# Optimization experiments

Hardware: AMD Instinct MI355X
Metric: run time of the kernel (lower is better)

The kernel has to match this reference:

```python
import jax, jax.numpy as jnp
import numpy as np

# SMPL constants and module defaults
NV, NF, T, S = 6890, 13776, 3, 256
NEAR, FAR = 0.1, 25.0
VIEW_ANGLE = 30.0
EYE = np.array([0.0, 0.0, -(1.0 / np.tan(np.radians(VIEW_ANGLE)) + 1.0)], np.float32)
AMB_INT, DIR_INT = 1.0, 0.0
AMB_COL = np.array([1.0, 1.0, 1.0], np.float32)
DIR_COL = np.array([1.0, 1.0, 1.0], np.float32)
LIGHT_DIR = np.array([0.0, 1.0, 0.0], np.float32)
BG = np.array([0.0, 0.0, 0.0], np.float32)
CHUNK = 128  # faces processed per z-buffer scan step


def _coords(t):
    # create_coords: (2, T*T) barycentric-style grid over [0,1]^2 (torch meshgrid 'ij')
    step = 1.0 / (t - 1) if t > 1 else 1.0
    ab = np.arange(0.0, 1.0 + step * 0.5, step, dtype=np.float32)
    xv, yv = np.meshgrid(ab, ab, indexing='ij')
    return jnp.asarray(np.stack([xv.ravel(), yv.ravel()], 0))

COORDS = _coords(T)


def _grid_sample(img, grid):
    # F.grid_sample: bilinear, zeros padding, align_corners=False
    # img (B,C,H,W), grid (B,N,M,2) in [-1,1] -> (B,C,N,M)
    Bc, C, H, W = img.shape
    gx = (grid[..., 0] + 1.0) * (W * 0.5) - 0.5
    gy = (grid[..., 1] + 1.0) * (H * 0.5) - 0.5
    x0 = jnp.floor(gx)
    y0 = jnp.floor(gy)
    fx = gx - x0
    fy = gy - y0

    def tap(xi, yi, w):
        valid = (xi >= 0) & (xi < W) & (yi >= 0) & (yi < H)
        xc = jnp.clip(xi, 0, W - 1).astype(jnp.int32)
        yc = jnp.clip(yi, 0, H - 1).astype(jnp.int32)
        v = jax.vmap(lambda im, y, x: im[:, y, x])(img, yc, xc)  # (B,C,N,M)
        return v * (w * valid)[:, None]

    return (tap(x0, y0, (1 - fx) * (1 - fy)) + tap(x0 + 1, y0, fx * (1 - fy))
            + tap(x0, y0 + 1, (1 - fx) * fy) + tap(x0 + 1, y0 + 1, fx * fy))


def _rasterize_one(f3, tex):
    # f3: (NF,3,3) camera-space face vertices (x,y in [-1,1] screen, z depth)
    # tex: (NF,T,T,T,3) per-face texture cube. Z-buffer rasterization (NMR-style,
    # CCW front faces only, perspective-correct depth and texture weights).
    F = f3.shape[0]
    pad = (-F) % CHUNK
    f3p = jnp.concatenate([f3, jnp.zeros((pad, 3, 3), f3.dtype)], 0)
    nc = f3p.shape[0] // CHUNK
    chunks = f3p.reshape(nc, CHUNK, 3, 3)
    bases = jnp.arange(nc, dtype=jnp.int32) * CHUNK
    yi, xi = jnp.meshgrid(jnp.arange(S), jnp.arange(S), indexing='ij')
    px = ((2.0 * xi.ravel() + 1.0 - S) / S).astype(f3.dtype)  # (P,)
    py = ((2.0 * yi.ravel() + 1.0 - S) / S).astype(f3.dtype)
    P = S * S

    @jax.checkpoint
    def step(carry, inp):
        zbuf, fid, wbuf = carry
        base, fc = inp
        vx = fc[:, :, 0][..., None]  # (C,3,1)
        vy = fc[:, :, 1][..., None]
        vz = fc[:, :, 2]             # (C,3)
        x0, x1, x2 = vx[:, 0], vx[:, 1], vx[:, 2]
        y0, y1, y2 = vy[:, 0], vy[:, 1], vy[:, 2]
        det = (x1 - x0) * (y2 - y0) - (y1 - y0) * (x2 - x0)  # (C,1)
        e0 = (x1 - px) * (y2 - py) - (y1 - py) * (x2 - px)   # (C,P)
        e1 = (x2 - px) * (y0 - py) - (y2 - py) * (x0 - px)
        e2 = (x0 - px) * (y1 - py) - (y0 - py) * (x1 - px)
        den = jnp.where(jnp.abs(det) > 1e-10, det, 1.0)
        b0, b1, b2 = e0 / den, e1 / den, e2 / den
        zs = jnp.where(jnp.abs(vz) > 1e-8, vz, 1.0)  # (C,3)
        inv_z = b0 / zs[:, 0:1] + b1 / zs[:, 1:2] + b2 / zs[:, 2:3]
        inv_z = jnp.where(jnp.abs(inv_z) > 1e-8, inv_z, 1.0)
        zp = 1.0 / inv_z  # perspective-correct depth at pixel
        inside = (det > 1e-10) & (e0 >= 0) & (e1 >= 0) & (e2 >= 0)
        valid = inside & (zp > NEAR) & (zp < FAR)
        zm = jnp.where(valid, zp, jnp.inf)
        best = jnp.argmin(zm, axis=0)  # (P,)
        bz = jnp.take_along_axis(zm, best[None], 0)[0]
        w = jnp.stack([jnp.take_along_axis(b0, best[None], 0)[0],
                       jnp.take_along_axis(b1, best[None], 0)[0],
                       jnp.take_along_axis(b2, best[None], 0)[0]], -1)  # (P,3)
        zv = zs[best]  # (P,3)
        bzf = jnp.where(jnp.isfinite(bz), bz, 0.0)
        wpc = (w / zv) * bzf[:, None]  # perspective-correct barycentric
        upd = bz < zbuf
        zbuf = jnp.where(upd, bz, zbuf)
        fid = jnp.where(upd, base + best.astype(jnp.int32), fid)
        wbuf = jnp.where(upd[:, None], wpc, wbuf)
        return (zbuf, fid, wbuf), None

    init = (jnp.full((P,), jnp.inf, f3.dtype),
            jnp.full((P,), -1, jnp.int32),
            jnp.zeros((P, 3), f3.dtype))
    (zbuf, fid, wbuf), _ = jax.lax.scan(step, init, (bases, chunks))

    # trilinear texture-cube sampling at barycentric position
    fg = fid >= 0
    fidc = jnp.clip(fid, 0, F - 1)
    pos = jnp.clip(wbuf, 0.0, 1.0) * (T - 1)  # (P,3)
    i0 = jnp.clip(jnp.floor(pos), 0, max(T - 2, 0)).astype(jnp.int32)
    fr = jnp.clip(pos - i0, 0.0, 1.0)
    col = jnp.zeros((P, 3), f3.dtype)
    for d0 in (0, 1):
        for d1 in (0, 1):
            for d2 in (0, 1):
                wgt = ((fr[:, 0] if d0 else 1 - fr[:, 0])
                       * (fr[:, 1] if d1 else 1 - fr[:, 1])
                       * (fr[:, 2] if d2 else 1 - fr[:, 2]))
                c = tex[fidc,
                        jnp.minimum(i0[:, 0] + d0, T - 1),
                        jnp.minimum(i0[:, 1] + d1, T - 1),
                        jnp.minimum(i0[:, 2] + d2, T - 1)]  # (P,3)
                col = col + wgt[:, None] * c
    img = jnp.where(fg[:, None], col, jnp.asarray(BG, f3.dtype))
    return img.reshape(S, S, 3).transpose(2, 0, 1)  # (3,S,S)


def _forward(cam, vertices, uv_imgs, faces):
    B = cam.shape[0]
    # --- dynamic_sampler: orthographic projection + per-face barycentric UV grid ---
    pts2d = cam[:, None, 0:1] * (vertices[:, :, :2] + cam[:, None, 1:3])  # (B,NV,2)
    f2pts = pts2d[:, faces]                                               # (B,NF,3,2)
    v2 = f2pts[:, :, 2]
    mat = jnp.stack([f2pts[:, :, 0] - v2, f2pts[:, :, 1] - v2], axis=-1)  # (B,NF,2,2)
    sampler = jnp.einsum('bfik,kt->bfti', mat, COORDS) + v2[:, :, None, :]
    sampler = jnp.clip(sampler, -1.0, 1.0)                                # (B,NF,T*T,2)
    # --- extract_tex ---
    tex = _grid_sample(uv_imgs, sampler)                                  # (B,3,NF,T*T)
    tex = tex.reshape(B, 3, NF, T, T).transpose(0, 2, 3, 4, 1)            # (B,NF,T,T,3)
    textures = jnp.repeat(tex[:, :, :, :, None, :], T, axis=4)            # (B,NF,T,T,T,3)
    # --- lighting (defaults: ambient=1, directional=0 -> identity; kept general) ---
    fverts = vertices[:, faces]  # (B,NF,3,3)
    n = jnp.cross(fverts[:, :, 1] - fverts[:, :, 0], fverts[:, :, 2] - fverts[:, :, 0])
    n = n / (jnp.linalg.norm(n, axis=-1, keepdims=True) + 1e-10)
    ldir = jnp.asarray(LIGHT_DIR / np.linalg.norm(LIGHT_DIR))
    cos = jax.nn.relu(n @ ldir)
    light = AMB_INT * jnp.asarray(AMB_COL) + DIR_INT * jnp.asarray(DIR_COL) * cos[..., None]
    tex_lit = textures * light[:, :, None, None, None, :]
    # --- projection (y flipped) + look_at ---
    proj = jnp.concatenate([pts2d[..., 0:1], -pts2d[..., 1:2], vertices[:, :, 2:3]], -1)
    eye = jnp.asarray(EYE)
    z_ax = -eye / jnp.linalg.norm(eye)
    x_ax = jnp.cross(jnp.array([0.0, 1.0, 0.0], proj.dtype), z_ax)
    x_ax = x_ax / jnp.linalg.norm(x_ax)
    y_ax = jnp.cross(z_ax, x_ax)
    R = jnp.stack([x_ax, y_ax, z_ax])  # (3,3)
    vcam = (proj - eye) @ R.T
    f3 = vcam[:, faces]  # (B,NF,3,3)
    images = jax.vmap(_rasterize_one)(f3, tex_lit)  # (B,3,S,S)
    return images, textures


def setup_inputs() -> dict:
    key = jax.random.key(0)
    k1, k2, k3, k4 = jax.random.split(key, 4)
    cam = jax.random.uniform(k1, (1, 3), dtype=jnp.float32)
    vertices = jax.random.normal(k2, (1, NV, 3), dtype=jnp.float32)
    uv_imgs = jax.random.uniform(k3, (1, 3, 256, 256), dtype=jnp.float32)
    faces = jax.random.randint(k4, (NF, 3), 0, NV, dtype=jnp.int32)
    return {"cam": cam, "vertices": vertices, "uv_imgs": uv_imgs, "faces": faces}


def reference(cam, vertices, uv_imgs, faces):
    return _forward(cam, vertices, uv_imgs, faces)
```

## Files before the change

kernel.cpp:

```cpp
#include <hip/hip_runtime.h>

#define NVERT 6890
#define NFACE 13776
#define SS 256
#define NPIX (SS*SS)
#define TILE 8
#define NSB 256
#define SPLIT 16
#define SEGLEN 861
#define SENTINEL 0xFFFFFFFFFFFFFFFFULL
#define ZBASE 0x3D000000u
#define EYEZ 2.7320508075688776f

#define OFF_KEYS 0u
#define OFF_FD   524288u
#define OFF_HIST 1405952u
#define OFF_CURS 1406976u
#define OFF_TD2  1408000u

static __device__ __forceinline__ unsigned int zbucket(unsigned int zmb) {
  return (zmb > ZBASE) ? min(255u, (zmb - ZBASE) >> 19) : 0u;
}

static __device__ __forceinline__ float edgef(float ax, float ay, float bx, float by,
                                              float px, float py) {
  return __fsub_rn(__fmul_rn(__fsub_rn(ax, px), __fsub_rn(by, py)),
                   __fmul_rn(__fsub_rn(ay, py), __fsub_rn(bx, px)));
}

__global__ __launch_bounds__(256) void tex_k(const float* __restrict__ cam,
                                             const float* __restrict__ verts,
                                             const int* __restrict__ faces,
                                             const float* __restrict__ uv,
                                             float* __restrict__ out_tex) {
  int tid = blockIdx.x * 256 + threadIdx.x;
  if (tid >= NFACE * 9) return;
  int f = tid / 9, t = tid - f * 9;
  int ti = t / 3, tj = t - ti * 3;
  float xt = 0.5f * (float)ti;
  float yt = 0.5f * (float)tj;
  float c0 = cam[0], c1 = cam[1], c2 = cam[2];
  int ia = faces[f*3+0], ib = faces[f*3+1], ic = faces[f*3+2];
  float ax = __fmul_rn(c0, __fadd_rn(verts[ia*3+0], c1));
  float ay = __fmul_rn(c0, __fadd_rn(verts[ia*3+1], c2));
  float bx = __fmul_rn(c0, __fadd_rn(verts[ib*3+0], c1));
  float by = __fmul_rn(c0, __fadd_rn(verts[ib*3+1], c2));
  float cx = __fmul_rn(c0, __fadd_rn(verts[ic*3+0], c1));
  float cy = __fmul_rn(c0, __fadd_rn(verts[ic*3+1], c2));
  float sx = (ax - cx) * xt + (bx - cx) * yt + cx;
  float sy = (ay - cy) * xt + (by - cy) * yt + cy;
  sx = fminf(fmaxf(sx, -1.f), 1.f);
  sy = fminf(fmaxf(sy, -1.f), 1.f);
  float gx = (sx + 1.f) * 128.f - 0.5f;
  float gy = (sy + 1.f) * 128.f - 0.5f;
  float x0f = floorf(gx), y0f = floorf(gy);
  float fx = gx - x0f, fy = gy - y0f;
  int x0 = (int)x0f, y0 = (int)y0f;
  float r = 0.f, g = 0.f, b = 0.f;
  #pragma unroll
  for (int dy = 0; dy < 2; ++dy) {
    #pragma unroll
    for (int dx = 0; dx < 2; ++dx) {
      int xi = x0 + dx, yi = y0 + dy;
      if (xi >= 0 && xi < SS && yi >= 0 && yi < SS) {
        float w = (dx ? fx : 1.f - fx) * (dy ? fy : 1.f - fy);
        int base = yi * SS + xi;
        r += w * uv[base];
        g += w * uv[NPIX + base];
        b += w * uv[2 * NPIX + base];
      }
    }
  }
  float* ot = out_tex + f * 81 + ti * 27 + tj * 9;
  #pragma unroll
  for (int kk = 0; kk < 3; ++kk) {
    ot[kk*3+0] = r; ot[kk*3+1] = g; ot[kk*3+2] = b;
  }
}

__global__ __launch_bounds__(256) void setup_k(const float* __restrict__ cam,
                                               const float* __restrict__ verts,
                                               const int* __restrict__ faces,
                                               float* __restrict__ fd,
                                               unsigned int* __restrict__ hist) {
  int f = blockIdx.x * 256 + threadIdx.x;
  if (f >= NFACE) return;
  float* fp = fd + (size_t)f * 16;
  float c0 = cam[0], c1 = cam[1], c2 = cam[2];
  int ia = faces[f*3+0], ib = faces[f*3+1], ic = faces[f*3+2];
  float x0 =  __fmul_rn(c0, __fadd_rn(verts[ia*3+0], c1));
  float y0 = -__fmul_rn(c0, __fadd_rn(verts[ia*3+1], c2));
  float z0 =  __fadd_rn(verts[ia*3+2], EYEZ);
  float x1 =  __fmul_rn(c0, __fadd_rn(verts[ib*3+0], c1));
  float y1 = -__fmul_rn(c0, __fadd_rn(verts[ib*3+1], c2));
  float z1 =  __fadd_rn(verts[ib*3+2], EYEZ);
  float x2 =  __fmul_rn(c0, __fadd_rn(verts[ic*3+0], c1));
  float y2 = -__fmul_rn(c0, __fadd_rn(verts[ic*3+1], c2));
  float z2 =  __fadd_rn(verts[ic*3+2], EYEZ);
  float det = edgef(x1, y1, x2, y2, x0, y0);
  unsigned int tilepack = 0x000000FFu;
  if (det > 1e-10f) {
    float mnx = fminf(x0, fminf(x1, x2)), mxx = fmaxf(x0, fmaxf(x1, x2));
    float mny = fminf(y0, fminf(y1, y2)), mxy = fmaxf(y0, fmaxf(y1, y2));
    int xlo = max((int)floorf((mnx * 256.f + 255.f) * 0.5f) - 2, 0);
    int xhi = min((int)ceilf ((mxx * 256.f + 255.f) * 0.5f) + 2, SS - 1);
    int ylo = max((int)floorf((mny * 256.f + 255.f) * 0.5f) - 2, 0);
    int yhi = min((int)ceilf ((mxy * 256.f + 255.f) * 0.5f) + 2, SS - 1);
    if (xlo <= xhi && ylo <= yhi)
      tilepack = (unsigned int)(xlo >> 3) | ((unsigned int)(ylo >> 3) << 8)
               | ((unsigned int)(xhi >> 3) << 16) | ((unsigned int)(yhi >> 3) << 24);
  }
  float rz0 = (fabsf(z0) > 1e-8f) ? z0 : 1.0f;
  float rz1 = (fabsf(z1) > 1e-8f) ? z1 : 1.0f;
  float rz2 = (fabsf(z2) > 1e-8f) ? z2 : 1.0f;
  float minrz = fminf(fminf(fabsf(rz0), fabsf(rz1)), fabsf(rz2));
  unsigned int flag = (minrz < 0.05f) ? 1u : 0u;
  unsigned int zmb = 0u;
  if (flag == 0u) {
    float mn = fminf(fminf(rz0, rz1), rz2);
    if (mn > 0.f) zmb = __float_as_uint(mn * 0.999f);
  }
  fp[0] = x0;  fp[1] = y0;  fp[2] = x1;  fp[3] = y1;
  fp[4] = x2;  fp[5] = y2;  fp[6] = rz0; fp[7] = rz1;
  fp[8] = rz2; fp[9] = det;
  fp[10] = __fdiv_rn(1.0f, det * rz0);
  fp[11] = __fdiv_rn(1.0f, det * rz1);
  fp[12] = __fdiv_rn(1.0f, det * rz2);
  fp[13] = __uint_as_float((unsigned int)f | (flag << 24));
  fp[14] = __uint_as_float(tilepack);
  fp[15] = __uint_as_float(zmb);
  atomicAdd(&hist[zbucket(zmb)], 1u);
}

__global__ __launch_bounds__(256) void scatter_k(const float* __restrict__ fd,
                                                 const unsigned int* __restrict__ hist,
                                                 unsigned int* __restrict__ curs,
                                                 uint4* __restrict__ td2) {
  __shared__ unsigned int bsh[256];
  int tid = threadIdx.x;
  unsigned int v = hist[tid];
  bsh[tid] = v;
  __syncthreads();
  for (int off = 1; off < 256; off <<= 1) {
    unsigned int t = (tid >= off) ? bsh[tid - off] : 0u;
    __syncthreads();
    bsh[tid] += t;
    __syncthreads();
  }
  int f = blockIdx.x * 256 + tid;
  if (f >= NFACE) return;
  const float* fp = fd + (size_t)f * 16;
  unsigned int tilepack = __float_as_uint(fp[14]);
  unsigned int zmb      = __float_as_uint(fp[15]);
  unsigned int b = zbucket(zmb);
  unsigned int slot = (bsh[b] - hist[b]) + atomicAdd(&curs[b], 1u);
  unsigned int pos = (slot & 15u) * SEGLEN + (slot >> 4);
  td2[pos] = make_uint4(tilepack, zmb, (unsigned int)f, 0u);
}

__global__ __launch_bounds__(256) void tile_k(const float* __restrict__ fd,
                                              const uint4* __restrict__ td2,
                                              unsigned long long* __restrict__ keys) {
  __shared__ unsigned short idx_s[4][256];
  __shared__ unsigned int cnt_s[4];
  __shared__ unsigned int wmax_s[4];
  int sb  = blockIdx.x & (NSB - 1);
  int seg = blockIdx.x >> 8;
  int tid = threadIdx.x;
  int w = tid >> 6, lane = tid & 63;
  int sbx = sb & 15, sby = sb >> 4;
  int tx = sbx * 2 + (w & 1);
  int ty = sby * 2 + (w >> 1);
  int xx = tx * TILE + (lane & 7);
  int yy = ty * TILE + (lane >> 3);
  float px = (float)(2 * xx + 1 - SS) * (1.0f / 256.0f);
  float py = (float)(2 * yy + 1 - SS) * (1.0f / 256.0f);
  int p = yy * SS + xx;
  unsigned long long best = SENTINEL;
  unsigned long long lastw = SENTINEL;
  const uint4* tseg = td2 + (size_t)seg * SEGLEN;

  for (int base = 0; base < SEGLEN; base += 256) {
    unsigned int gz = (unsigned int)(keys[p] >> 32);
    unsigned int kz = min((unsigned int)(best >> 32), gz);
    unsigned int bh = kz;
    #pragma unroll
    for (int o = 32; o > 0; o >>= 1)
      bh = max(bh, (unsigned int)__shfl_xor((int)bh, o, 64));
    __syncthreads();
    if (lane == 0) wmax_s[w] = bh;
    if (tid < 4) cnt_s[tid] = 0;
    __syncthreads();
    unsigned int bm = max(max(wmax_s[0], wmax_s[1]), max(wmax_s[2], wmax_s[3]));
    unsigned int z0 = tseg[base].y;
    unsigned int b0 = zbucket(z0);
    unsigned int lb = b0 ? (ZBASE + (b0 << 19)) : 0u;
    if (lb > bm) break;
    int fi = base + tid;
    if (fi < SEGLEN) {
      uint4 t2 = tseg[fi];
      unsigned int tp = t2.x, zmb = t2.y;
      int tx0 = (int)(tp & 255u),         ty0 = (int)((tp >> 8) & 255u);
      int tx1 = (int)((tp >> 16) & 255u), ty1 = (int)(tp >> 24);
      #pragma unroll
      for (int q = 0; q < 4; ++q) {
        int qtx = sbx * 2 + (q & 1);
        int qty = sby * 2 + (q >> 1);
        if (qtx >= tx0 && qtx <= tx1 && qty >= ty0 && qty <= ty1
            && zmb <= wmax_s[q]) {
          unsigned int slot = atomicAdd(&cnt_s[q], 1u);
          idx_s[q][slot] = (unsigned short)t2.z;
        }
      }
    }
    __syncthreads();
    int m = (int)cnt_s[w];
    for (int j = 0; j < m; ++j) {
      int f2 = __builtin_amdgcn_readfirstlane((int)idx_s[w][j]);
      const float4* fr = (const float4*)(fd + (size_t)f2 * 16);
      float4 A  = fr[0];
      float4 Bv = fr[1];
      float4 Cv = fr[2];
      float4 Dv = fr[3];
      unsigned int zmb = __float_as_uint(Dv.w);
      if (zmb > kz) continue;
      float e0 = edgef(A.z, A.w, Bv.x, Bv.y, px, py);
      float e1 = edgef(Bv.x, Bv.y, A.x, A.y, px, py);
      float e2 = edgef(A.x, A.y, A.z, A.w, px, py);
      if (e0 >= 0.f && e1 >= 0.f && e2 >= 0.f) {
        float inva = __fmaf_rn(e0, Cv.z, __fmaf_rn(e1, Cv.w, e2 * Dv.x));
        float zc = __uint_as_float(kz);
        unsigned int w13 = __float_as_uint(Dv.y);
        bool pass = (kz >= 0x7F800000u)
                  | ((w13 >> 24) != 0u) | (inva * zc > 0.998f) | (fabsf(inva) < 1e-4f);
        if (pass) {
          float rz0 = Bv.z, rz1 = Bv.w, rz2 = Cv.x, det = Cv.y;
          float b0f = __fdiv_rn(e0, det);
          float b1f = __fdiv_rn(e1, det);
          float b2f = __fdiv_rn(e2, det);
          float inv = __fadd_rn(__fadd_rn(__fdiv_rn(b0f, rz0), __fdiv_rn(b1f, rz1)),
                                __fdiv_rn(b2f, rz2));
          if (!(fabsf(inv) > 1e-8f)) inv = 1.0f;
          float zp = __fdiv_rn(1.0f, inv);
          if (zp > 0.1f && zp < 25.0f) {
            unsigned long long key =
                ((unsigned long long)__float_as_uint(zp) << 32)
                | (w13 & 0x00FFFFFFu);
            if (key < best) {
              best = key;
              kz = min(kz, (unsigned int)(best >> 32));
            }
          }
        }
      }
    }
    if (best != lastw && (unsigned int)(best >> 32) <= gz) {
      atomicMin(&keys[p], best);
      lastw = best;
    }
  }
}

__global__ __launch_bounds__(256) void resolve_k(const float* __restrict__ cam,
                                                 const float* __restrict__ verts,
                                                 const int* __restrict__ faces,
                                                 const unsigned long long* __restrict__ keys,
                                                 const float* __restrict__ out_tex,
                                                 float* __restrict__ out_img) {
  int p = blockIdx.x * 256 + threadIdx.x;
  if (p >= NPIX) return;
  unsigned long long k = keys[p];
  float c0v = 0.f, c1v = 0.f, c2v = 0.f;
  if (k != SENTINEL) {
    int f = (int)(unsigned int)(k & 0x00FFFFFFULL);
    float bz = __uint_as_float((unsigned int)(k >> 32));
    int xx = p & (SS - 1), yy = p >> 8;
    float px = (float)(2 * xx + 1 - SS) * (1.0f / 256.0f);
    float py = (float)(2 * yy + 1 - SS) * (1.0f / 256.0f);
    float c0 = cam[0], c1 = cam[1], c2 = cam[2];
    int ia = faces[f*3+0], ib = faces[f*3+1], ic = faces[f*3+2];
    float x0 =  __fmul_rn(c0, __fadd_rn(verts[ia*3+0], c1));
    float y0 = -__fmul_rn(c0, __fadd_rn(verts[ia*3+1], c2));
    float z0 =  __fadd_rn(verts[ia*3+2], EYEZ);
    float x1 =  __fmul_rn(c0, __fadd_rn(verts[ib*3+0], c1));
    float y1 = -__fmul_rn(c0, __fadd_rn(verts[ib*3+1], c2));
    float z1 =  __fadd_rn(verts[ib*3+2], EYEZ);
    float x2 =  __fmul_rn(c0, __fadd_rn(verts[ic*3+0], c1));
    float y2 = -__fmul_rn(c0, __fadd_rn(verts[ic*3+1], c2));
    float z2 =  __fadd_rn(verts[ic*3+2], EYEZ);
    float det = edgef(x1, y1, x2, y2, x0, y0);
    float e0 = edgef(x1, y1, x2, y2, px, py);
    float e1 = edgef(x2, y2, x0, y0, px, py);
    float e2 = edgef(x0, y0, x1, y1, px, py);
    float b0 = __fdiv_rn(e0, det);
    float b1 = __fdiv_rn(e1, det);
    float b2 = __fdiv_rn(e2, det);
    float rz0 = (fabsf(z0) > 1e-8f) ? z0 : 1.0f;
    float rz1 = (fabsf(z1) > 1e-8f) ? z1 : 1.0f;
    float rz2 = (fabsf(z2) > 1e-8f) ? z2 : 1.0f;
    float w0 = __fmul_rn(__fdiv_rn(b0, rz0), bz);
    float w1 = __fmul_rn(__fdiv_rn(b1, rz1), bz);
    float w2 = __fmul_rn(__fdiv_rn(b2, rz2), bz);
    float pos0 = fminf(fmaxf(w0, 0.f), 1.f) * 2.f;
    float pos1 = fminf(fmaxf(w1, 0.f), 1.f) * 2.f;
    float pos2 = fminf(fmaxf(w2, 0.f), 1.f) * 2.f;
    float i0f = fminf(fmaxf(floorf(pos0), 0.f), 1.f);
    float i1f = fminf(fmaxf(floorf(pos1), 0.f), 1.f);
    float i2f = fminf(fmaxf(floorf(pos2), 0.f), 1.f);
    float fr0 = fminf(fmaxf(__fsub_rn(pos0, i0f), 0.f), 1.f);
    float fr1 = fminf(fmaxf(__fsub_rn(pos1, i1f), 0.f), 1.f);
    float fr2 = fminf(fmaxf(__fsub_rn(pos2, i2f), 0.f), 1.f);
    int i00 = (int)i0f, i01 = (int)i1f;
    #pragma unroll
    for (int d0 = 0; d0 < 2; ++d0) {
      float wa = d0 ? fr0 : __fsub_rn(1.f, fr0);
      #pragma unroll
      for (int d1 = 0; d1 < 2; ++d1) {
        float wb = d1 ? fr1 : __fsub_rn(1.f, fr1);
        int a = min(i00 + d0, 2);
        int b = min(i01 + d1, 2);
        const float* tp = &out_tex[f * 81 + a * 27 + b * 9];
        float wab = __fmul_rn(wa, wb);
        #pragma unroll
        for (int d2 = 0; d2 < 2; ++d2) {
          float wc = d2 ? fr2 : __fsub_rn(1.f, fr2);
          float wgt = __fmul_rn(wab, wc);
          c0v = __fadd_rn(c0v, __fmul_rn(wgt, tp[0]));
          c1v = __fadd_rn(c1v, __fmul_rn(wgt, tp[1]));
          c2v = __fadd_rn(c2v, __fmul_rn(wgt, tp[2]));
        }
      }
    }
  }
  out_img[p]          = c0v;
  out_img[NPIX + p]   = c1v;
  out_img[2*NPIX + p] = c2v;
}

extern "C" void kernel_launch(void* const* d_in, const int* in_sizes, int n_in,
                              void* d_out, int out_size, void* d_ws, size_t ws_size,
                              hipStream_t stream) {
  const float* cam   = (const float*)d_in[0];
  const float* verts = (const float*)d_in[1];
  const float* uv    = (const float*)d_in[2];
  const int*   faces = (const int*)d_in[3];
  float* out_img = (float*)d_out;
  float* out_tex = (float*)d_out + 3 * NPIX;

  char* ws = (char*)d_ws;
  unsigned long long* keys = (unsigned long long*)(ws + OFF_KEYS);
  float* fd          = (float*)(ws + OFF_FD);
  unsigned int* hist = (unsigned int*)(ws + OFF_HIST);
  unsigned int* curs = (unsigned int*)(ws + OFF_CURS);
  uint4* td2         = (uint4*)(ws + OFF_TD2);

  hipMemsetAsync(keys, 0xFF, (size_t)NPIX * 8, stream);
  hipMemsetAsync(hist, 0, 2048, stream);
  setup_k<<<(NFACE + 255) / 256, 256, 0, stream>>>(cam, verts, faces, fd, hist);
  tex_k<<<(NFACE * 9 + 255) / 256, 256, 0, stream>>>(cam, verts, faces, uv, out_tex);
  scatter_k<<<(NFACE + 255) / 256, 256, 0, stream>>>(fd, hist, curs, td2);
  tile_k<<<NSB * SPLIT, 256, 0, stream>>>(fd, td2, keys);
  resolve_k<<<NPIX / 256, 256, 0, stream>>>(cam, verts, faces, keys, out_tex, out_img);
}
```

Baseline: 191.7 us.

## Fuse setup, texture and key init into one prep kernel with per-block histograms

Merges face setup, texture sampling and the key-buffer sentinel fill into a single prep kernel, removing two memsets and two launches. Each setup block builds a local shared-memory depth-bucket histogram and writes it out, so there are no global atomics on a shared histogram. A single 1024-thread block then reduces the partial histograms, scans them, and scatters faces using shared-memory cursors. That also removes the old global cursor array, which was never reset between calls. The conservative depth-pass threshold in the tile kernel is loosened from 0.998 to 0.995, so more candidates go through the exact depth test; this trades a little extra work for safety. The single-block scatter is serial over all faces and may lengthen that stage.

```diff
diff --git a/kernel.cpp b/kernel.cpp
--- a/kernel.cpp
+++ b/kernel.cpp
@@ -8,15 +8,15 @@
 #define NSB 256
 #define SPLIT 16
 #define SEGLEN 861
+#define NSETUPBLK 54
 #define SENTINEL 0xFFFFFFFFFFFFFFFFULL
 #define ZBASE 0x3D000000u
 #define EYEZ 2.7320508075688776f
 
 #define OFF_KEYS 0u
 #define OFF_FD   524288u
-#define OFF_HIST 1405952u
-#define OFF_CURS 1406976u
-#define OFF_TD2  1408000u
+#define OFF_PH   1405952u
+#define OFF_TD2  1461248u
 
 static __device__ __forceinline__ unsigned int zbucket(unsigned int zmb) {
   return (zmb > ZBASE) ? min(255u, (zmb - ZBASE) >> 19) : 0u;
@@ -28,134 +28,162 @@
                    __fmul_rn(__fsub_rn(ay, py), __fsub_rn(bx, px)));
 }
 
-__global__ __launch_bounds__(256) void tex_k(const float* __restrict__ cam,
-                                             const float* __restrict__ verts,
-                                             const int* __restrict__ faces,
-                                             const float* __restrict__ uv,
-                                             float* __restrict__ out_tex) {
-  int tid = blockIdx.x * 256 + threadIdx.x;
-  if (tid >= NFACE * 9) return;
-  int f = tid / 9, t = tid - f * 9;
-  int ti = t / 3, tj = t - ti * 3;
-  float xt = 0.5f * (float)ti;
-  float yt = 0.5f * (float)tj;
+__global__ __launch_bounds__(256) void prep_k(const float* __restrict__ cam,
+                                              const float* __restrict__ verts,
+                                              const int* __restrict__ faces,
+                                              const float* __restrict__ uv,
+                                              float* __restrict__ fd,
+                                              unsigned int* __restrict__ phist,
+                                              unsigned long long* __restrict__ keys,
+                                              float* __restrict__ out_tex) {
+  __shared__ unsigned int lh[256];
+  int blk = blockIdx.x;
+  int tid = threadIdx.x;
+  int i = blk * 256 + tid;
+  bool hblk = (blk < NSETUPBLK);
+  if (hblk) lh[tid] = 0u;
+  if (i < NPIX) keys[i] = SENTINEL;
   float c0 = cam[0], c1 = cam[1], c2 = cam[2];
-  int ia = faces[f*3+0], ib = faces[f*3+1], ic = faces[f*3+2];
-  float ax = __fmul_rn(c0, __fadd_rn(verts[ia*3+0], c1));
-  float ay = __fmul_rn(c0, __fadd_rn(verts[ia*3+1], c2));
-  float bx = __fmul_rn(c0, __fadd_rn(verts[ib*3+0], c1));
-  float by = __fmul_rn(c0, __fadd_rn(verts[ib*3+1], c2));
-  float cx = __fmul_rn(c0, __fadd_rn(verts[ic*3+0], c1));
-  float cy = __fmul_rn(c0, __fadd_rn(verts[ic*3+1], c2));
-  float sx = (ax - cx) * xt + (bx - cx) * yt + cx;
-  float sy = (ay - cy) * xt + (by - cy) * yt + cy;
-  sx = fminf(fmaxf(sx, -1.f), 1.f);
-  sy = fminf(fmaxf(sy, -1.f), 1.f);
-  float gx = (sx + 1.f) * 128.f - 0.5f;
-  float gy = (sy + 1.f) * 128.f - 0.5f;
-  float x0f = floorf(gx), y0f = floorf(gy);
-  float fx = gx - x0f, fy = gy - y0f;
-  int x0 = (int)x0f, y0 = (int)y0f;
-  float r = 0.f, g = 0.f, b = 0.f;
-  #pragma unroll
-  for (int dy = 0; dy < 2; ++dy) {
+
+  unsigned int mybucket = 0u;
+  bool isface = (i < NFACE);
+  if (isface) {
+    int f = i;
+    float* fp = fd + (size_t)f * 16;
+    int ia = faces[f*3+0], ib = faces[f*3+1], ic = faces[f*3+2];
+    float x0 =  __fmul_rn(c0, __fadd_rn(verts[ia*3+0], c1));
+    float y0 = -__fmul_rn(c0, __fadd_rn(verts[ia*3+1], c2));
+    float z0 =  __fadd_rn(verts[ia*3+2], EYEZ);
+    float x1 =  __fmul_rn(c0, __fadd_rn(verts[ib*3+0], c1));
+    float y1 = -__fmul_rn(c0, __fadd_rn(verts[ib*3+1], c2));
+    float z1 =  __fadd_rn(verts[ib*3+2], EYEZ);
+    float x2 =  __fmul_rn(c0, __fadd_rn(verts[ic*3+0], c1));
+    float y2 = -__fmul_rn(c0, __fadd_rn(verts[ic*3+1], c2));
+    float z2 =  __fadd_rn(verts[ic*3+2], EYEZ);
+    float det = edgef(x1, y1, x2, y2, x0, y0);
+    unsigned int tilepack = 0x000000FFu;
+    if (det > 1e-10f) {
+      float mnx = fminf(x0, fminf(x1, x2)), mxx = fmaxf(x0, fmaxf(x1, x2));
+      float mny = fminf(y0, fminf(y1, y2)), mxy = fmaxf(y0, fmaxf(y1, y2));
+      int xlo = max((int)floorf((mnx * 256.f + 255.f) * 0.5f) - 2, 0);
+      int xhi = min((int)ceilf ((mxx * 256.f + 255.f) * 0.5f) + 2, SS - 1);
+      int ylo = max((int)floorf((mny * 256.f + 255.f) * 0.5f) - 2, 0);
+      int yhi = min((int)ceilf ((mxy * 256.f + 255.f) * 0.5f) + 2, SS - 1);
+      if (xlo <= xhi && ylo <= yhi)
+        tilepack = (unsigned int)(xlo >> 3) | ((unsigned int)(ylo >> 3) << 8)
+                 | ((unsigned int)(xhi >> 3) << 16) | ((unsigned int)(yhi >> 3) << 24);
+    }
+    float rz0 = (fabsf(z0) > 1e-8f) ? z0 : 1.0f;
+    float rz1 = (fabsf(z1) > 1e-8f) ? z1 : 1.0f;
+    float rz2 = (fabsf(z2) > 1e-8f) ? z2 : 1.0f;
+    float minrz = fminf(fminf(fabsf(rz0), fabsf(rz1)), fabsf(rz2));
+    unsigned int flag = (minrz < 0.05f) ? 1u : 0u;
+    unsigned int zmb = 0u;
+    if (flag == 0u) {
+      float mn = fminf(fminf(rz0, rz1), rz2);
+      if (mn > 0.f) zmb = __float_as_uint(mn * 0.999f);
+    }
+    fp[0] = x0;  fp[1] = y0;  fp[2] = x1;  fp[3] = y1;
+    fp[4] = x2;  fp[5] = y2;  fp[6] = rz0; fp[7] = rz1;
+    fp[8] = rz2; fp[9] = det;
+    fp[10] = __fdiv_rn(1.0f, det * rz0);
+    fp[11] = __fdiv_rn(1.0f, det * rz1);
+    fp[12] = __fdiv_rn(1.0f, det * rz2);
+    fp[13] = __uint_as_float((unsigned int)f | (flag << 24));
+    fp[14] = __uint_as_float(tilepack);
+    fp[15] = __uint_as_float(zmb);
+    mybucket = zbucket(zmb);
+  }
+  if (hblk) {
+    __syncthreads();
+    if (isface) atomicAdd(&lh[mybucket], 1u);
+    __syncthreads();
+    phist[blk * 256 + tid] = lh[tid];
+  }
+
+  if (i < NFACE * 9) {
+    int f = i / 9, t = i - f * 9;
+    int ti = t / 3, tj = t - ti * 3;
+    float xt = 0.5f * (float)ti;
+    float yt = 0.5f * (float)tj;
+    int ia = faces[f*3+0], ib = faces[f*3+1], ic = faces[f*3+2];
+    float ax = __fmul_rn(c0, __fadd_rn(verts[ia*3+0], c1));
+    float ay = __fmul_rn(c0, __fadd_rn(verts[ia*3+1], c2));
+    float bx = __fmul_rn(c0, __fadd_rn(verts[ib*3+0], c1));
+    float by = __fmul_rn(c0, __fadd_rn(verts[ib*3+1], c2));
+    float cx = __fmul_rn(c0, __fadd_rn(verts[ic*3+0], c1));
+    float cy = __fmul_rn(c0, __fadd_rn(verts[ic*3+1], c2));
+    float sx = (ax - cx) * xt + (bx - cx) * yt + cx;
+    float sy = (ay - cy) * xt + (by - cy) * yt + cy;
+    sx = fminf(fmaxf(sx, -1.f), 1.f);
+    sy = fminf(fmaxf(sy, -1.f), 1.f);
+    float gx = (sx + 1.f) * 128.f - 0.5f;
+    float gy = (sy + 1.f) * 128.f - 0.5f;
+    float x0f = floorf(gx), y0f = floorf(gy);
+    float fx = gx - x0f, fy = gy - y0f;
+    int x0 = (int)x0f, y0 = (int)y0f;
+    float r = 0.f, g = 0.f, b = 0.f;
     #pragma unroll
-    for (int dx = 0; dx < 2; ++dx) {
-      int xi = x0 + dx, yi = y0 + dy;
-      if (xi >= 0 && xi < SS && yi >= 0 && yi < SS) {
-        float w = (dx ? fx : 1.f - fx) * (dy ? fy : 1.f - fy);
-        int base = yi * SS + xi;
-        r += w * uv[base];
-        g += w * uv[NPIX + base];
-        b += w * uv[2 * NPIX + base];
+    for (int dy = 0; dy < 2; ++dy) {
+      #pragma unroll
+      for (int dx = 0; dx < 2; ++dx) {
+        int xi = x0 + dx, yi = y0 + dy;
+        if (xi >= 0 && xi < SS && yi >= 0 && yi < SS) {
+          float w = (dx ? fx : 1.f - fx) * (dy ? fy : 1.f - fy);
+          int base = yi * SS + xi;
+          r += w * uv[base];
+          g += w * uv[NPIX + base];
+          b += w * uv[2 * NPIX + base];
+        }
       }
     }
-  }
-  float* ot = out_tex + f * 81 + ti * 27 + tj * 9;
-  #pragma unroll
-  for (int kk = 0; kk < 3; ++kk) {
-    ot[kk*3+0] = r; ot[kk*3+1] = g; ot[kk*3+2] = b;
-  }
-}
-
-__global__ __launch_bounds__(256) void setup_k(const float* __restrict__ cam,
-                                               const float* __restrict__ verts,
-                                               const int* __restrict__ faces,
-                                               float* __restrict__ fd,
-                                               unsigned int* __restrict__ hist) {
-  int f = blockIdx.x * 256 + threadIdx.x;
-  if (f >= NFACE) return;
-  float* fp = fd + (size_t)f * 16;
-  float c0 = cam[0], c1 = cam[1], c2 = cam[2];
-  int ia = faces[f*3+0], ib = faces[f*3+1], ic = faces[f*3+2];
-  float x0 =  __fmul_rn(c0, __fadd_rn(verts[ia*3+0], c1));
-  float y0 = -__fmul_rn(c0, __fadd_rn(verts[ia*3+1], c2));
-  float z0 =  __fadd_rn(verts[ia*3+2], EYEZ);
-  float x1 =  __fmul_rn(c0, __fadd_rn(verts[ib*3+0], c1));
-  float y1 = -__fmul_rn(c0, __fadd_rn(verts[ib*3+1], c2));
-  float z1 =  __fadd_rn(verts[ib*3+2], EYEZ);
-  float x2 =  __fmul_rn(c0, __fadd_rn(verts[ic*3+0], c1));
-  float y2 = -__fmul_rn(c0, __fadd_rn(verts[ic*3+1], c2));
-  float z2 =  __fadd_rn(verts[ic*3+2], EYEZ);
-  float det = edgef(x1, y1, x2, y2, x0, y0);
-  unsigned int tilepack = 0x000000FFu;
-  if (det > 1e-10f) {
-    float mnx = fminf(x0, fminf(x1, x2)), mxx = fmaxf(x0, fmaxf(x1, x2));
-    float mny = fminf(y0, fminf(y1, y2)), mxy = fmaxf(y0, fmaxf(y1, y2));
-    int xlo = max((int)floorf((mnx * 256.f + 255.f) * 0.5f) - 2, 0);
-    int xhi = min((int)ceilf ((mxx * 256.f + 255.f) * 0.5f) + 2, SS - 1);
-    int ylo = max((int)floorf((mny * 256.f + 255.f) * 0.5f) - 2, 0);
-    int yhi = min((int)ceilf ((mxy * 256.f + 255.f) * 0.5f) + 2, SS - 1);
-    if (xlo <= xhi && ylo <= yhi)
-      tilepack = (unsigned int)(xlo >> 3) | ((unsigned int)(ylo >> 3) << 8)
-               | ((unsigned int)(xhi >> 3) << 16) | ((unsigned int)(yhi >> 3) << 24);
-  }
-  float rz0 = (fabsf(z0) > 1e-8f) ? z0 : 1.0f;
-  float rz1 = (fabsf(z1) > 1e-8f) ? z1 : 1.0f;
-  float rz2 = (fabsf(z2) > 1e-8f) ? z2 : 1.0f;
-  float minrz = fminf(fminf(fabsf(rz0), fabsf(rz1)), fabsf(rz2));
-  unsigned int flag = (minrz < 0.05f) ? 1u : 0u;
-  unsigned int zmb = 0u;
-  if (flag == 0u) {
-    float mn = fminf(fminf(rz0, rz1), rz2);
-    if (mn > 0.f) zmb = __float_as_uint(mn * 0.999f);
-  }
-  fp[0] = x0;  fp[1] = y0;  fp[2] = x1;  fp[3] = y1;
-  fp[4] = x2;  fp[5] = y2;  fp[6] = rz0; fp[7] = rz1;
-  fp[8] = rz2; fp[9] = det;
-  fp[10] = __fdiv_rn(1.0f, det * rz0);
-  fp[11] = __fdiv_rn(1.0f, det * rz1);
-  fp[12] = __fdiv_rn(1.0f, det * rz2);
-  fp[13] = __uint_as_float((unsigned int)f | (flag << 24));
-  fp[14] = __uint_as_float(tilepack);
-  fp[15] = __uint_as_float(zmb);
-  atomicAdd(&hist[zbucket(zmb)], 1u);
-}
-
-__global__ __launch_bounds__(256) void scatter_k(const float* __restrict__ fd,
-                                                 const unsigned int* __restrict__ hist,
-                                                 unsigned int* __restrict__ curs,
-                                                 uint4* __restrict__ td2) {
-  __shared__ unsigned int bsh[256];
+    float* ot = out_tex + f * 81 + ti * 27 + tj * 9;
+    #pragma unroll
+    for (int kk = 0; kk < 3; ++kk) {
+      ot[kk*3+0] = r; ot[kk*3+1] = g; ot[kk*3+2] = b;
+    }
+  }
+}
+
+__global__ __launch_bounds__(1024) void scatter_k(const float* __restrict__ fd,
+                                                  const unsigned int* __restrict__ phist,
+                                                  uint4* __restrict__ td2) {
+  __shared__ unsigned int part[1024];
+  __shared__ unsigned int sc[256];
+  __shared__ unsigned int excl[256];
+  __shared__ unsigned int curs[256];
   int tid = threadIdx.x;
-  unsigned int v = hist[tid];
-  bsh[tid] = v;
+  unsigned int b255 = (unsigned int)(tid & 255), strip = (unsigned int)(tid >> 8);
+  unsigned int s = 0;
+  for (unsigned int bb = strip; bb < NSETUPBLK; bb += 4)
+    s += phist[bb * 256 + b255];
+  part[tid] = s;
+  __syncthreads();
+  unsigned int v = 0;
+  if (tid < 256) {
+    v = part[tid] + part[tid + 256] + part[tid + 512] + part[tid + 768];
+    sc[tid] = v;
+    curs[tid] = 0u;
+  }
   __syncthreads();
   for (int off = 1; off < 256; off <<= 1) {
-    unsigned int t = (tid >= off) ? bsh[tid - off] : 0u;
-    __syncthreads();
-    bsh[tid] += t;
-    __syncthreads();
-  }
-  int f = blockIdx.x * 256 + tid;
-  if (f >= NFACE) return;
-  const float* fp = fd + (size_t)f * 16;
-  unsigned int tilepack = __float_as_uint(fp[14]);
-  unsigned int zmb      = __float_as_uint(fp[15]);
-  unsigned int b = zbucket(zmb);
-  unsigned int slot = (bsh[b] - hist[b]) + atomicAdd(&curs[b], 1u);
-  unsigned int pos = (slot & 15u) * SEGLEN + (slot >> 4);
-  td2[pos] = make_uint4(tilepack, zmb, (unsigned int)f, 0u);
+    unsigned int t_ = 0;
+    if (tid < 256 && tid >= off) t_ = sc[tid - off];
+    __syncthreads();
+    if (tid < 256) sc[tid] += t_;
+    __syncthreads();
+  }
+  if (tid < 256) excl[tid] = sc[tid] - v;
+  __syncthreads();
+  for (int f = tid; f < NFACE; f += 1024) {
+    const float* fp = fd + (size_t)f * 16;
+    unsigned int tilepack = __float_as_uint(fp[14]);
+    unsigned int zmb      = __float_as_uint(fp[15]);
+    unsigned int b = zbucket(zmb);
+    unsigned int slot = excl[b] + atomicAdd(&curs[b], 1u);
+    unsigned int pos = (slot & 15u) * SEGLEN + (slot >> 4);
+    td2[pos] = make_uint4(tilepack, zmb, (unsigned int)f, 0u);
+  }
 }
 
 __global__ __launch_bounds__(256) void tile_k(const float* __restrict__ fd,
@@ -232,7 +260,7 @@
         float zc = __uint_as_float(kz);
         unsigned int w13 = __float_as_uint(Dv.y);
         bool pass = (kz >= 0x7F800000u)
-                  | ((w13 >> 24) != 0u) | (inva * zc > 0.998f) | (fabsf(inva) < 1e-4f);
+                  | ((w13 >> 24) != 0u) | (inva * zc > 0.995f) | (fabsf(inva) < 1e-4f);
         if (pass) {
           float rz0 = Bv.z, rz1 = Bv.w, rz2 = Cv.x, det = Cv.y;
           float b0f = __fdiv_rn(e0, det);
@@ -349,16 +377,13 @@
 
   char* ws = (char*)d_ws;
   unsigned long long* keys = (unsigned long long*)(ws + OFF_KEYS);
-  float* fd          = (float*)(ws + OFF_FD);
-  unsigned int* hist = (unsigned int*)(ws + OFF_HIST);
-  unsigned int* curs = (unsigned int*)(ws + OFF_CURS);
-  uint4* td2         = (uint4*)(ws + OFF_TD2);
-
-  hipMemsetAsync(keys, 0xFF, (size_t)NPIX * 8, stream);
-  hipMemsetAsync(hist, 0, 2048, stream);
-  setup_k<<<(NFACE + 255) / 256, 256, 0, stream>>>(cam, verts, faces, fd, hist);
-  tex_k<<<(NFACE * 9 + 255) / 256, 256, 0, stream>>>(cam, verts, faces, uv, out_tex);
-  scatter_k<<<(NFACE + 255) / 256, 256, 0, stream>>>(fd, hist, curs, td2);
+  float* fd           = (float*)(ws + OFF_FD);
+  unsigned int* phist = (unsigned int*)(ws + OFF_PH);
+  uint4* td2          = (uint4*)(ws + OFF_TD2);
+
+  prep_k<<<(NFACE * 9 + 255) / 256, 256, 0, stream>>>(cam, verts, faces, uv,
+                                                      fd, phist, keys, out_tex);
+  scatter_k<<<1, 1024, 0, stream>>>(fd, phist, td2);
   tile_k<<<NSB * SPLIT, 256, 0, stream>>>(fd, td2, keys);
   resolve_k<<<NPIX / 256, 256, 0, stream>>>(cam, verts, faces, keys, out_tex, out_img);
 }
```

After: 164.6 us. -14.2%, faster.
